# Performance work log

Measured on AMD Instinct MI355X. Metric: run time of the kernel, lower is better.

## Reference

```python
import jax, jax.numpy as jnp
import numpy as np

D_MODEL = 4096
N_HEADS = 32
KV_HEADS = 8
HEAD_DIM = D_MODEL // N_HEADS  # 128
GROUPS = N_HEADS // KV_HEADS   # 4
ROPE_THETA = 500000.0
CLIP_QKV = 8.0
SEQLENS = [512, 768, 384, 384]
T = sum(SEQLENS)  # 2048 total ragged tokens


def setup_inputs() -> dict:
    key = jax.random.key(0)
    k1, k2, k3 = jax.random.split(key, 3)
    hidden_states = jax.random.normal(k1, (T, D_MODEL), dtype=jnp.float32)
    # fused Wqkv: rows = d_model (Q) + 2 * kv_heads * head_dim (K,V)
    w_qkv = jax.random.normal(k2, (D_MODEL + 2 * KV_HEADS * HEAD_DIM, D_MODEL), dtype=jnp.float32) * 0.02
    w_o = jax.random.normal(k3, (D_MODEL, D_MODEL), dtype=jnp.float32) * 0.02
    # ragged-batch metadata: cumulative sequence lengths, per-token positions
    cu = np.concatenate([[0], np.cumsum(SEQLENS)]).astype(np.int32)
    pos = np.concatenate([np.arange(l) for l in SEQLENS]).astype(np.float32)
    inv_freq = 1.0 / (ROPE_THETA ** (np.arange(0, HEAD_DIM, 2, dtype=np.float32) / HEAD_DIM))  # [64]
    freqs = pos[:, None] * inv_freq[None, :]  # [T, 64]
    return {
        "hidden_states": hidden_states,
        "w_qkv": w_qkv,
        "w_o": w_o,
        "cos": jnp.asarray(np.cos(freqs), dtype=jnp.float32),
        "sin": jnp.asarray(np.sin(freqs), dtype=jnp.float32),
        "cu_seqlens": jnp.asarray(cu),
    }


def _rope(x, cos, sin):
    # rotate-half (NeoX-style) RoPE, as in TGI PositionRotaryEmbedding
    h = HEAD_DIM // 2
    x1, x2 = x[..., :h], x[..., h:]
    c = cos[:, None, :]  # [T,1,h] broadcast over heads
    s = sin[:, None, :]
    return jnp.concatenate([x1 * c - x2 * s, x2 * c + x1 * s], axis=-1)


def reference(hidden_states, w_qkv, w_o, cos, sin, cu_seqlens):
    # fused QKV projection + clip_qkv clamp
    qkv = jnp.clip(hidden_states @ w_qkv.T, -CLIP_QKV, CLIP_QKV)  # [T, 6144]
    q_sz = N_HEADS * HEAD_DIM
    kv_sz = KV_HEADS * HEAD_DIM
    q = qkv[:, :q_sz].reshape(T, N_HEADS, HEAD_DIM)
    k = qkv[:, q_sz:q_sz + kv_sz].reshape(T, KV_HEADS, HEAD_DIM)
    v = qkv[:, q_sz + kv_sz:].reshape(T, KV_HEADS, HEAD_DIM)
    q = _rope(q, cos, sin)
    k = _rope(k, cos, sin)
    # GQA: expand kv heads to query heads (kv_head_mapping = repeat_interleave)
    kr = jnp.repeat(k, GROUPS, axis=1)  # [T, H, D]
    vr = jnp.repeat(v, GROUPS, axis=1)
    # varlen causal mask: same segment AND key index <= query index
    idx = jnp.arange(T)
    seg = jnp.searchsorted(cu_seqlens, idx, side="right") - 1  # [T]
    mask = (seg[:, None] == seg[None, :]) & (idx[:, None] >= idx[None, :])  # [T,T]
    scale = HEAD_DIM ** -0.5
    scores = jnp.einsum("qhd,khd->hqk", q, kr) * scale  # [H,T,T]
    scores = jnp.where(mask[None, :, :], scores, jnp.finfo(scores.dtype).min)
    attn = jax.nn.softmax(scores, axis=-1)
    out = jnp.einsum("hqk,khd->qhd", attn, vr).reshape(T, N_HEADS * HEAD_DIM)
    return out @ w_o.T
```

## Files before the change

### kernel.cpp

```cpp
#include <hip/hip_runtime.h>

#define T_TOK 2048
#define DM    4096
#define NH    32
#define KVH   8
#define HD    128
#define QKV_N 6144
#define KOFF  4096
#define VOFF  5120
#define SCALE 0.08838834764831845f

typedef __attribute__((ext_vector_type(8))) short  short8;
typedef __attribute__((ext_vector_type(4))) float  floatx4;

__device__ __forceinline__ ushort f2bf(float f) {
  union { float f; unsigned u; } x; x.f = f;
  unsigned u = x.u;
  return (ushort)((u + 0x7fffu + ((u >> 16) & 1u)) >> 16);
}
__device__ __forceinline__ float bf2f(ushort h) {
  union { unsigned u; float f; } x; x.u = ((unsigned)h) << 16;
  return x.f;
}

__global__ void __launch_bounds__(256) cast_bf16_kernel(const float* __restrict__ x,
                                                        ushort* __restrict__ y, int n4) {
  int i = blockIdx.x * 256 + threadIdx.x;
  if (i >= n4) return;
  float4 v = ((const float4*)x)[i];
  ushort4 o;
  o.x = f2bf(v.x); o.y = f2bf(v.y); o.z = f2bf(v.z); o.w = f2bf(v.w);
  ((ushort4*)y)[i] = o;
}

__device__ __forceinline__ void gld_lds16(const ushort* g, ushort* l) {
  __builtin_amdgcn_global_load_lds((const __attribute__((address_space(1))) unsigned int*)g,
                                   (__attribute__((address_space(3))) unsigned int*)l,
                                   16, 0, 0);
}

__global__ void __launch_bounds__(256) gemm_bt(const ushort* __restrict__ A,
                                               const ushort* __restrict__ B,
                                               ushort* __restrict__ Cb,
                                               float* __restrict__ Cf,
                                               int N, int K, int mode) {
  __shared__ ushort As[128 * 32];
  __shared__ ushort Bs[128 * 32];
  const int tid = threadIdx.x, wave = tid >> 6, lane = tid & 63;
  const int bm = blockIdx.y * 128, bn = blockIdx.x * 128;
  const int wr = (wave >> 1) * 64, wc = (wave & 1) * 64;
  const int r = lane & 15, g = lane >> 4;

  floatx4 zero = {0.f, 0.f, 0.f, 0.f};
  floatx4 acc[4][4];
#pragma unroll
  for (int mi = 0; mi < 4; mi++)
#pragma unroll
    for (int ni = 0; ni < 4; ni++) acc[mi][ni] = zero;

  const ushort* Ag = A + (size_t)(bm + wave * 32 + (lane >> 2)) * K + (lane & 3) * 8;
  const ushort* Bg = B + (size_t)(bn + wave * 32 + (lane >> 2)) * K + (lane & 3) * 8;
  ushort* Al = &As[(wave * 32) * 32];
  ushort* Bl = &Bs[(wave * 32) * 32];

  for (int k0 = 0; k0 < K; k0 += 32) {
    gld_lds16(Ag,          Al);
    gld_lds16(Ag + 16 * K, Al + 16 * 32);
    gld_lds16(Bg,          Bl);
    gld_lds16(Bg + 16 * K, Bl + 16 * 32);
    Ag += 32; Bg += 32;
    __syncthreads();

    short8 af[4], bfr[4];
#pragma unroll
    for (int i = 0; i < 4; i++) af[i]  = *(const short8*)&As[(wr + i * 16 + r) * 32 + g * 8];
#pragma unroll
    for (int i = 0; i < 4; i++) bfr[i] = *(const short8*)&Bs[(wc + i * 16 + r) * 32 + g * 8];
#pragma unroll
    for (int mi = 0; mi < 4; mi++)
#pragma unroll
      for (int ni = 0; ni < 4; ni++)
        acc[mi][ni] = __builtin_amdgcn_mfma_f32_16x16x32_bf16(af[mi], bfr[ni], acc[mi][ni], 0, 0, 0);
    __syncthreads();
  }

#pragma unroll
  for (int mi = 0; mi < 4; mi++)
#pragma unroll
    for (int v = 0; v < 4; v++) {
      int row = bm + wr + mi * 16 + g * 4 + v;
#pragma unroll
      for (int ni = 0; ni < 4; ni++) {
        int col = bn + wc + ni * 16 + r;
        float x = acc[mi][ni][v];
        if (mode == 0) {
          x = fminf(8.0f, fmaxf(-8.0f, x));
          Cb[(size_t)row * N + col] = f2bf(x);
        } else {
          Cf[(size_t)row * N + col] = x;
        }
      }
    }
}

__global__ void __launch_bounds__(256) rope_kernel(ushort* __restrict__ qkv,
                                                   const float* __restrict__ cosb,
                                                   const float* __restrict__ sinb) {
  int t = blockIdx.y;
  int h = blockIdx.x * 4 + (threadIdx.x >> 6);
  int d = threadIdx.x & 63;
  size_t base = (size_t)t * QKV_N + (h < NH ? h * HD : KOFF + (h - NH) * HD);
  float x1 = bf2f(qkv[base + d]);
  float x2 = bf2f(qkv[base + 64 + d]);
  float c = cosb[t * 64 + d], s = sinb[t * 64 + d];
  float y1 = x1 * c - x2 * s;
  float y2 = x2 * c + x1 * s;
  if (h < NH) { y1 *= SCALE; y2 *= SCALE; }
  qkv[base + d]      = f2bf(y1);
  qkv[base + 64 + d] = f2bf(y2);
}

__global__ void __launch_bounds__(256) vtrans_kernel(const ushort* __restrict__ qkv,
                                                     ushort* __restrict__ vt) {
  int idx = blockIdx.x * 256 + threadIdx.x;
  int t  = idx & (T_TOK - 1);
  int d  = (idx >> 11) & (HD - 1);
  int kv = idx >> 18;
  vt[idx] = qkv[(size_t)t * QKV_N + VOFF + kv * HD + d];
}

__global__ void __launch_bounds__(256) attn_kernel(const ushort* __restrict__ qkv,
                                                   const ushort* __restrict__ vt,
                                                   ushort* __restrict__ o) {
  __shared__ ushort Ks[64][136];
  __shared__ ushort Vts[128][72];
  __shared__ ushort Ps[4][16][72];

  const int tid = threadIdx.x, wave = tid >> 6, lane = tid & 63;
  const int r = lane & 15, g = lane >> 4;
  const int qtile = blockIdx.x, head = blockIdx.y, kvh = head >> 2;
  const int q0 = qtile * 64;
  int s0;
  if (q0 < 512) s0 = 0; else if (q0 < 1280) s0 = 512;
  else if (q0 < 1664) s0 = 1280; else s0 = 1664;

  short8 qf[4];
  const int qrow = q0 + wave * 16 + r;
#pragma unroll
  for (int ks = 0; ks < 4; ks++)
    qf[ks] = *(const short8*)&qkv[(size_t)qrow * QKV_N + head * HD + ks * 32 + g * 8];

  floatx4 zero = {0.f, 0.f, 0.f, 0.f};
  floatx4 oacc[8];
#pragma unroll
  for (int b = 0; b < 8; b++) oacc[b] = zero;
  float mrun[4] = {-1e30f, -1e30f, -1e30f, -1e30f};
  float lrun[4] = {0.f, 0.f, 0.f, 0.f};

  const size_t kcol  = (size_t)KOFF + kvh * HD;
  const size_t vbase = (size_t)kvh * HD * T_TOK;

  for (int k0 = s0; k0 < q0 + 64; k0 += 64) {
    short8 kreg[4], vreg[4];
#pragma unroll
    for (int p = 0; p < 4; p++) {
      int krow = p * 16 + (tid >> 4), kc = (tid & 15) * 8;
      kreg[p] = *(const short8*)&qkv[(size_t)(k0 + krow) * QKV_N + kcol + kc];
      int vd = p * 32 + (tid >> 3), vc = (tid & 7) * 8;
      vreg[p] = *(const short8*)&vt[vbase + (size_t)vd * T_TOK + k0 + vc];
    }
    __syncthreads();
#pragma unroll
    for (int p = 0; p < 4; p++) {
      int krow = p * 16 + (tid >> 4), kc = (tid & 15) * 8;
      *(short8*)&Ks[krow][kc] = kreg[p];
      int vd = p * 32 + (tid >> 3), vc = (tid & 7) * 8;
      *(short8*)&Vts[vd][vc] = vreg[p];
    }
    __syncthreads();

    floatx4 sacc[4];
#pragma unroll
    for (int s = 0; s < 4; s++) sacc[s] = zero;
#pragma unroll
    for (int s = 0; s < 4; s++)
#pragma unroll
      for (int ks = 0; ks < 4; ks++) {
        short8 kf = *(const short8*)&Ks[s * 16 + r][ks * 32 + g * 8];
        sacc[s] = __builtin_amdgcn_mfma_f32_16x16x32_bf16(qf[ks], kf, sacc[s], 0, 0, 0);
      }

    const bool diag = (k0 == q0);
    float sv[4][4];
#pragma unroll
    for (int s = 0; s < 4; s++)
#pragma unroll
      for (int v = 0; v < 4; v++) {
        float x = sacc[s][v];
        if (diag) {
          int ka = k0 + s * 16 + r;
          int qa = q0 + wave * 16 + g * 4 + v;
          if (ka > qa) x = -1e30f;
        }
        sv[s][v] = x;
      }

    float rmax[4];
#pragma unroll
    for (int v = 0; v < 4; v++)
      rmax[v] = fmaxf(fmaxf(sv[0][v], sv[1][v]), fmaxf(sv[2][v], sv[3][v]));
#pragma unroll
    for (int off = 1; off < 16; off <<= 1)
#pragma unroll
      for (int v = 0; v < 4; v++)
        rmax[v] = fmaxf(rmax[v], __shfl_xor(rmax[v], off, 64));

    float newm[4], alpha[4];
#pragma unroll
    for (int v = 0; v < 4; v++) {
      newm[v]  = fmaxf(mrun[v], rmax[v]);
      alpha[v] = __expf(mrun[v] - newm[v]);
      mrun[v]  = newm[v];
    }

    float pv[4][4];
    float rsum[4] = {0.f, 0.f, 0.f, 0.f};
#pragma unroll
    for (int s = 0; s < 4; s++)
#pragma unroll
      for (int v = 0; v < 4; v++) {
        float p = __expf(sv[s][v] - newm[v]);
        pv[s][v] = p;
        rsum[v] += p;
      }
#pragma unroll
    for (int off = 1; off < 16; off <<= 1)
#pragma unroll
      for (int v = 0; v < 4; v++)
        rsum[v] += __shfl_xor(rsum[v], off, 64);
#pragma unroll
    for (int v = 0; v < 4; v++) lrun[v] = lrun[v] * alpha[v] + rsum[v];
#pragma unroll
    for (int b = 0; b < 8; b++)
#pragma unroll
      for (int v = 0; v < 4; v++) oacc[b][v] *= alpha[v];

#pragma unroll
    for (int s = 0; s < 4; s++)
#pragma unroll
      for (int v = 0; v < 4; v++)
        Ps[wave][g * 4 + v][s * 16 + r] = f2bf(pv[s][v]);
    __syncthreads();

    short8 pf0 = *(const short8*)&Ps[wave][r][g * 8];
    short8 pf1 = *(const short8*)&Ps[wave][r][32 + g * 8];

#pragma unroll
    for (int b = 0; b < 8; b++) {
      short8 v0 = *(const short8*)&Vts[b * 16 + r][g * 8];
      short8 v1 = *(const short8*)&Vts[b * 16 + r][32 + g * 8];
      oacc[b] = __builtin_amdgcn_mfma_f32_16x16x32_bf16(pf0, v0, oacc[b], 0, 0, 0);
      oacc[b] = __builtin_amdgcn_mfma_f32_16x16x32_bf16(pf1, v1, oacc[b], 0, 0, 0);
    }
  }

  float rinv[4];
#pragma unroll
  for (int v = 0; v < 4; v++) rinv[v] = 1.0f / lrun[v];
#pragma unroll
  for (int b = 0; b < 8; b++)
#pragma unroll
    for (int v = 0; v < 4; v++) {
      int qa = q0 + wave * 16 + g * 4 + v;
      o[(size_t)qa * DM + head * HD + b * 16 + r] = f2bf(oacc[b][v] * rinv[v]);
    }
}

extern "C" void kernel_launch(void* const* d_in, const int* in_sizes, int n_in,
                              void* d_out, int out_size, void* d_ws, size_t ws_size,
                              hipStream_t stream) {
  const float* hs   = (const float*)d_in[0];
  const float* wqkv = (const float*)d_in[1];
  const float* wo   = (const float*)d_in[2];
  const float* cosb = (const float*)d_in[3];
  const float* sinb = (const float*)d_in[4];
  float* out = (float*)d_out;

  char* w = (char*)d_ws;
  ushort* h_bf   = (ushort*)(w);
  ushort* wq_bf  = (ushort*)(w + 16777216);
  ushort* wo_bf  = (ushort*)(w + 67108864);
  ushort* qkv_bf = (ushort*)(w + 100663296);
  ushort* vt     = (ushort*)(w + 125829120);
  ushort* ao_bf  = (ushort*)(w + 130023424);

  cast_bf16_kernel<<<8192,  256, 0, stream>>>(hs,   h_bf,  2097152);
  cast_bf16_kernel<<<24576, 256, 0, stream>>>(wqkv, wq_bf, 6291456);
  cast_bf16_kernel<<<16384, 256, 0, stream>>>(wo,   wo_bf, 4194304);

  gemm_bt<<<dim3(48, 16), 256, 0, stream>>>(h_bf, wq_bf, qkv_bf, nullptr, QKV_N, DM, 0);
  rope_kernel<<<dim3(10, T_TOK), 256, 0, stream>>>(qkv_bf, cosb, sinb);
  vtrans_kernel<<<8192, 256, 0, stream>>>(qkv_bf, vt);
  attn_kernel<<<dim3(32, 32), 256, 0, stream>>>(qkv_bf, vt, ao_bf);
  gemm_bt<<<dim3(32, 16), 256, 0, stream>>>(ao_bf, wo_bf, nullptr, out, DM, DM, 1);
}
```

Baseline: 560.5 us.

## Read K/V fragments directly from global memory and tile the V transpose

The attention kernel drops its shared-memory staging of K and V tiles and the two block barriers per key tile. Each wave now loads its MFMA operand fragments straight from global memory and relies on L1/L2 for reuse across the four waves. The barrier between writing and reading the per-wave P buffer is also removed, since only the owning wave uses that buffer. Separately, the V transpose kernel becomes a 64x64 shared-memory tiled transpose with vector loads and stores, replacing the strided scalar gather. The risk is more global and L2 traffic plus higher load latency in the attention inner loop, traded for fewer synchronizations and less LDS use.

```diff
diff --git a/kernel.cpp b/kernel.cpp
--- a/kernel.cpp
+++ b/kernel.cpp
@@ -122,18 +122,31 @@
 
 __global__ void __launch_bounds__(256) vtrans_kernel(const ushort* __restrict__ qkv,
                                                      ushort* __restrict__ vt) {
-  int idx = blockIdx.x * 256 + threadIdx.x;
-  int t  = idx & (T_TOK - 1);
-  int d  = (idx >> 11) & (HD - 1);
-  int kv = idx >> 18;
-  vt[idx] = qkv[(size_t)t * QKV_N + VOFF + kv * HD + d];
+  __shared__ ushort tile[64][72];
+  const int tid = threadIdx.x;
+  const int t0 = blockIdx.x * 64, d0 = blockIdx.y * 64, kv = blockIdx.z;
+
+  {
+    int t = tid >> 2, c = (tid & 3) * 16;
+    const ushort* src = &qkv[(size_t)(t0 + t) * QKV_N + VOFF + kv * HD + d0 + c];
+    *(short8*)&tile[t][c]     = *(const short8*)(src);
+    *(short8*)&tile[t][c + 8] = *(const short8*)(src + 8);
+  }
+  __syncthreads();
+  {
+    int d = tid >> 2, c = (tid & 3) * 16;
+    ushort tmp[16];
+#pragma unroll
+    for (int j = 0; j < 16; j++) tmp[j] = tile[c + j][d];
+    ushort* dst = &vt[((size_t)kv * HD + d0 + d) * T_TOK + t0 + c];
+    *(short8*)(dst)     = *(const short8*)&tmp[0];
+    *(short8*)(dst + 8) = *(const short8*)&tmp[8];
+  }
 }
 
 __global__ void __launch_bounds__(256) attn_kernel(const ushort* __restrict__ qkv,
                                                    const ushort* __restrict__ vt,
                                                    ushort* __restrict__ o) {
-  __shared__ ushort Ks[64][136];
-  __shared__ ushort Vts[128][72];
   __shared__ ushort Ps[4][16][72];
 
   const int tid = threadIdx.x, wave = tid >> 6, lane = tid & 63;
@@ -157,38 +170,22 @@
   float mrun[4] = {-1e30f, -1e30f, -1e30f, -1e30f};
   float lrun[4] = {0.f, 0.f, 0.f, 0.f};
 
-  const size_t kcol  = (size_t)KOFF + kvh * HD;
-  const size_t vbase = (size_t)kvh * HD * T_TOK;
+  const ushort* Kb = qkv + KOFF + (size_t)kvh * HD;
+  const ushort* Vb = vt + (size_t)kvh * HD * T_TOK;
 
   for (int k0 = s0; k0 < q0 + 64; k0 += 64) {
-    short8 kreg[4], vreg[4];
-#pragma unroll
-    for (int p = 0; p < 4; p++) {
-      int krow = p * 16 + (tid >> 4), kc = (tid & 15) * 8;
-      kreg[p] = *(const short8*)&qkv[(size_t)(k0 + krow) * QKV_N + kcol + kc];
-      int vd = p * 32 + (tid >> 3), vc = (tid & 7) * 8;
-      vreg[p] = *(const short8*)&vt[vbase + (size_t)vd * T_TOK + k0 + vc];
-    }
-    __syncthreads();
-#pragma unroll
-    for (int p = 0; p < 4; p++) {
-      int krow = p * 16 + (tid >> 4), kc = (tid & 15) * 8;
-      *(short8*)&Ks[krow][kc] = kreg[p];
-      int vd = p * 32 + (tid >> 3), vc = (tid & 7) * 8;
-      *(short8*)&Vts[vd][vc] = vreg[p];
-    }
-    __syncthreads();
-
     floatx4 sacc[4];
 #pragma unroll
     for (int s = 0; s < 4; s++) sacc[s] = zero;
 #pragma unroll
-    for (int s = 0; s < 4; s++)
+    for (int s = 0; s < 4; s++) {
+      const ushort* krow = Kb + (size_t)(k0 + s * 16 + r) * QKV_N;
 #pragma unroll
       for (int ks = 0; ks < 4; ks++) {
-        short8 kf = *(const short8*)&Ks[s * 16 + r][ks * 32 + g * 8];
+        short8 kf = *(const short8*)(krow + ks * 32 + g * 8);
         sacc[s] = __builtin_amdgcn_mfma_f32_16x16x32_bf16(qf[ks], kf, sacc[s], 0, 0, 0);
       }
+    }
 
     const bool diag = (k0 == q0);
     float sv[4][4];
@@ -250,15 +247,15 @@
 #pragma unroll
       for (int v = 0; v < 4; v++)
         Ps[wave][g * 4 + v][s * 16 + r] = f2bf(pv[s][v]);
-    __syncthreads();
 
     short8 pf0 = *(const short8*)&Ps[wave][r][g * 8];
     short8 pf1 = *(const short8*)&Ps[wave][r][32 + g * 8];
 
 #pragma unroll
     for (int b = 0; b < 8; b++) {
-      short8 v0 = *(const short8*)&Vts[b * 16 + r][g * 8];
-      short8 v1 = *(const short8*)&Vts[b * 16 + r][32 + g * 8];
+      const ushort* vrow = Vb + (size_t)(b * 16 + r) * T_TOK + k0;
+      short8 v0 = *(const short8*)(vrow + g * 8);
+      short8 v1 = *(const short8*)(vrow + 32 + g * 8);
       oacc[b] = __builtin_amdgcn_mfma_f32_16x16x32_bf16(pf0, v0, oacc[b], 0, 0, 0);
       oacc[b] = __builtin_amdgcn_mfma_f32_16x16x32_bf16(pf1, v1, oacc[b], 0, 0, 0);
     }
@@ -300,7 +297,7 @@
 
   gemm_bt<<<dim3(48, 16), 256, 0, stream>>>(h_bf, wq_bf, qkv_bf, nullptr, QKV_N, DM, 0);
   rope_kernel<<<dim3(10, T_TOK), 256, 0, stream>>>(qkv_bf, cosb, sinb);
-  vtrans_kernel<<<8192, 256, 0, stream>>>(qkv_bf, vt);
+  vtrans_kernel<<<dim3(32, 2, 8), 256, 0, stream>>>(qkv_bf, vt);
   attn_kernel<<<dim3(32, 32), 256, 0, stream>>>(qkv_bf, vt, ao_bf);
   gemm_bt<<<dim3(32, 16), 256, 0, stream>>>(ao_bf, wo_bf, nullptr, out, DM, DM, 1);
 }
```

New measurement: 655.0 us. 1.17x slower.
